# Kernel tuning notes

Measured on AMD Instinct MI355X. Metric: run time of the kernel, lower is better.

The kernel has to match this reference:

```python
import jax, jax.numpy as jnp
import numpy as np

B, S, D, H = 2, 2048, 1024, 16
HD = D // H  # head dim = 64; scale uses sqrt(d_k/num_heads) = sqrt(D/H) since d_k==d_model


def setup_inputs() -> dict:
    key = jax.random.key(0)
    ks = jax.random.split(key, 12)
    s = 1.0 / np.sqrt(D)
    inp = {
        "Q": jax.random.normal(ks[0], (B, S, D), jnp.float32),
        "K": jax.random.normal(ks[1], (B, S, D), jnp.float32),
        "V": jax.random.normal(ks[2], (B, S, D), jnp.float32),
        "mask": jnp.tril(jnp.ones((S, S), jnp.int32))[None, None],  # [1,1,S,S] causal
        "Wq": jax.random.normal(ks[3], (D, D), jnp.float32) * s,
        "bq": jnp.zeros((D,), jnp.float32),
        "Wk": jax.random.normal(ks[4], (D, D), jnp.float32) * s,
        "bk": jnp.zeros((D,), jnp.float32),
        "Wv": jax.random.normal(ks[5], (D, D), jnp.float32) * s,
        "bv": jnp.zeros((D,), jnp.float32),
        "Wo": jax.random.normal(ks[6], (D, D), jnp.float32) * s,
        "bo": jnp.zeros((D,), jnp.float32),
    }
    return inp


def _split_heads(x):
    # [B,S,D] -> [B,H,S,HD]
    b, s, _ = x.shape
    return x.reshape(b, s, H, HD).transpose(0, 2, 1, 3)


def reference(Q, K, V, mask, Wq, bq, Wk, bk, Wv, bv, Wo, bo):
    q = _split_heads(Q @ Wq.T + bq)
    k = _split_heads(K @ Wk.T + bk)
    v = _split_heads(V @ Wv.T + bv)
    scale = 1.0 / jnp.sqrt(jnp.asarray(D / H, q.dtype))  # d_k/num_heads with d_k=d_model
    scores = jnp.einsum('bhqd,bhkd->bhqk', q, k) * scale
    scores = jnp.where(mask == 0, jnp.asarray(-1e9, scores.dtype), scores)
    probs = jax.nn.softmax(scores, axis=-1)
    z = jnp.einsum('bhqk,bhkd->bhqd', probs, v)  # [B,H,S,HD]
    z = z.transpose(0, 2, 1, 3).reshape(Q.shape[0], Q.shape[1], D)
    return z @ Wo.T + bo
```

## Files before the change

### kernel.cpp

```cpp
#include <hip/hip_runtime.h>
#include <hip/hip_bf16.h>

typedef unsigned short u16;
typedef unsigned int u32;
typedef __attribute__((ext_vector_type(2))) unsigned int u32x2;
typedef __attribute__((ext_vector_type(8))) short s16x8;
typedef __attribute__((ext_vector_type(4))) float f32x4;
typedef __attribute__((ext_vector_type(16))) float f32x16;

#define NB 2
#define NH 16
#define NS 2048
#define ND 1024
#define QSCALE 0.1803368801111244f

#define AS1(p) ((const __attribute__((address_space(1))) void*)(p))
#define AS3(p) ((__attribute__((address_space(3))) void*)(p))

__device__ __forceinline__ u16 f2bf(float f) {
  u32 u = __float_as_uint(f);
  u = u + 0x7FFFu + ((u >> 16) & 1u);
  return (u16)(u >> 16);
}

__device__ __forceinline__ float bf2f(u16 h) {
  return __uint_as_float(((u32)h) << 16);
}

__device__ __forceinline__ u32 pkbf(float a, float b) {
  __hip_bfloat162 h = __float22bfloat162_rn(make_float2(a, b));
  union { __hip_bfloat162 h; u32 u; } cv;
  cv.h = h;
  return cv.u;
}

__global__ __launch_bounds__(256) void cvt_kernel(
    const float* __restrict__ q, const float* __restrict__ k,
    const float* __restrict__ v, const float* __restrict__ wq,
    const float* __restrict__ wk, const float* __restrict__ wv,
    const float* __restrict__ wo, u16* __restrict__ Xbf,
    u16* __restrict__ Wbf) {
  const int s = blockIdx.z;
  const size_t M1 = (size_t)1024 * 1024;
  const float* src;
  u16* dst;
  if (s < 4)       { src = q + (size_t)s * M1;        dst = Xbf + (size_t)s * M1; }
  else if (s < 8)  { src = k + (size_t)(s - 4) * M1;  dst = Xbf + (size_t)s * M1; }
  else if (s < 12) { src = v + (size_t)(s - 8) * M1;  dst = Xbf + (size_t)s * M1; }
  else if (s == 12){ src = wq; dst = Wbf; }
  else if (s == 13){ src = wk; dst = Wbf + M1; }
  else if (s == 14){ src = wv; dst = Wbf + 2 * M1; }
  else             { src = wo; dst = Wbf + 3 * M1; }
  const int n4 = 1024 * 1024 / 4;
  for (int i = blockIdx.x * 256 + threadIdx.x; i < n4; i += gridDim.x * 256) {
    float4 a = ((const float4*)src)[i];
    uint2 p;
    p.x = (u32)f2bf(a.x) | ((u32)f2bf(a.y) << 16);
    p.y = (u32)f2bf(a.z) | ((u32)f2bf(a.w) << 16);
    ((uint2*)dst)[i] = p;
  }
}

__global__ __launch_bounds__(256) void gemm_qkv_fast(
    const u16* __restrict__ Xbf, const u16* __restrict__ Wbf,
    const float* __restrict__ bq, const float* __restrict__ bk,
    const float* __restrict__ bv, u16* __restrict__ qh, u16* __restrict__ kh,
    u16* __restrict__ vT) {
  const int which = blockIdx.z;
  const int m0 = blockIdx.y * 128, n0 = blockIdx.x * 128;
  const u16* A = Xbf + (size_t)which * 4096 * 1024;
  const u16* B = Wbf + (size_t)which * 1024 * 1024;
  const float* bias = (which == 0) ? bq : (which == 1) ? bk : bv;
  const int tid = threadIdx.x;
  const int w = tid >> 6, l = tid & 63, lr = l & 15, lg = l >> 4;
  const int wr = (w >> 1) * 64, wc = (w & 1) * 64;

  __shared__ u16 As[2][128 * 32];
  __shared__ u16 Bs[2][128 * 32];

  const int c0 = tid, c1 = 256 + tid;
  const int row0 = c0 >> 2, k40 = (c0 & 3) ^ (row0 & 3);
  const int row1 = c1 >> 2, k41 = (c1 & 3) ^ (row1 & 3);
  const u16* sa0 = A + (size_t)(m0 + row0) * 1024 + k40 * 8;
  const u16* sb0 = B + (size_t)(n0 + row0) * 1024 + k40 * 8;
  const u16* sa1 = A + (size_t)(m0 + row1) * 1024 + k41 * 8;
  const u16* sb1 = B + (size_t)(n0 + row1) * 1024 + k41 * 8;
  const int d0 = (w * 64) * 8, d1 = (256 + w * 64) * 8;

  const f32x4 fzero = {0.f, 0.f, 0.f, 0.f};
  f32x4 acc[4][4];
#pragma unroll
  for (int m = 0; m < 4; ++m)
#pragma unroll
    for (int n = 0; n < 4; ++n) acc[m][n] = fzero;

  auto STAGE = [&](int buf, int k0) {
    __builtin_amdgcn_global_load_lds(AS1(sa0 + k0), AS3(As[buf] + d0), 16, 0, 0);
    __builtin_amdgcn_global_load_lds(AS1(sb0 + k0), AS3(Bs[buf] + d0), 16, 0, 0);
    __builtin_amdgcn_global_load_lds(AS1(sa1 + k0), AS3(As[buf] + d1), 16, 0, 0);
    __builtin_amdgcn_global_load_lds(AS1(sb1 + k0), AS3(Bs[buf] + d1), 16, 0, 0);
  };

  STAGE(0, 0);
  STAGE(1, 32);
  asm volatile("s_waitcnt vmcnt(4)" ::: "memory");
  __builtin_amdgcn_sched_barrier(0);
  __builtin_amdgcn_s_barrier();

  int cur = 0;
  for (int step = 0; step < 32; ++step) {
    s16x8 af[4], bf[4];
#pragma unroll
    for (int m = 0; m < 4; ++m) {
      int row = wr + m * 16 + lr;
      af[m] = *(const s16x8*)(As[cur] + row * 32 + ((lg ^ (row & 3)) * 8));
    }
#pragma unroll
    for (int n = 0; n < 4; ++n) {
      int row = wc + n * 16 + lr;
      bf[n] = *(const s16x8*)(Bs[cur] + row * 32 + ((lg ^ (row & 3)) * 8));
    }
    asm volatile("s_waitcnt lgkmcnt(0)" ::: "memory");
    __builtin_amdgcn_sched_barrier(0);
    __builtin_amdgcn_s_barrier();

    const bool stg = (step + 2 < 32);
    if (stg) STAGE(cur, (step + 2) * 32);

    __builtin_amdgcn_s_setprio(1);
#pragma unroll
    for (int m = 0; m < 4; ++m)
#pragma unroll
      for (int n = 0; n < 4; ++n)
        acc[m][n] = __builtin_amdgcn_mfma_f32_16x16x32_bf16(af[m], bf[n],
                                                            acc[m][n], 0, 0, 0);
    __builtin_amdgcn_s_setprio(0);

    if (stg)
      asm volatile("s_waitcnt vmcnt(4)" ::: "memory");
    else
      asm volatile("s_waitcnt vmcnt(0)" ::: "memory");
    __builtin_amdgcn_sched_barrier(0);
    __builtin_amdgcn_s_barrier();
    cur ^= 1;
  }

#pragma unroll
  for (int m = 0; m < 4; ++m) {
#pragma unroll
    for (int n = 0; n < 4; ++n) {
#pragma unroll
      for (int i = 0; i < 4; ++i) {
        int row = m0 + wr + m * 16 + 4 * lg + i;
        int col = n0 + wc + n * 16 + lr;
        float val = acc[m][n][i] + bias[col];
        if (which == 0) val *= QSCALE;
        int bbi = row >> 11, ss = row & 2047;
        int hhd = col >> 6, hd = col & 63;
        if (which == 0) {
          qh[(((size_t)bbi * NH + hhd) * NS + ss) * 64 + hd] = f2bf(val);
        } else if (which == 1) {
          kh[(((size_t)bbi * NH + hhd) * NS + ss) * 64 + hd] = f2bf(val);
        } else {
          vT[(((size_t)bbi * NH + hhd) * 64 + hd) * NS + ss] = f2bf(val);
        }
      }
    }
  }
}

__global__ __launch_bounds__(256) void gemm_out_fast(
    const u16* __restrict__ zin, const u16* __restrict__ Wbf,
    const float* __restrict__ bo, float* __restrict__ out) {
  const u16* B = Wbf + (size_t)3 * 1024 * 1024;
  const int m0 = blockIdx.y * 128, n0 = blockIdx.x * 128;
  const int tid = threadIdx.x;
  const int w = tid >> 6, l = tid & 63, lr = l & 15, lg = l >> 4;
  const int wr = (w >> 1) * 64, wc = (w & 1) * 64;

  __shared__ u16 As[2][128 * 32];
  __shared__ u16 Bs[2][128 * 32];

  const int c0 = tid, c1 = 256 + tid;
  const int row0 = c0 >> 2, k40 = (c0 & 3) ^ (row0 & 3);
  const int row1 = c1 >> 2, k41 = (c1 & 3) ^ (row1 & 3);
  const u16* sa0 = zin + (size_t)(m0 + row0) * 1024 + k40 * 8;
  const u16* sb0 = B + (size_t)(n0 + row0) * 1024 + k40 * 8;
  const u16* sa1 = zin + (size_t)(m0 + row1) * 1024 + k41 * 8;
  const u16* sb1 = B + (size_t)(n0 + row1) * 1024 + k41 * 8;
  const int d0 = (w * 64) * 8, d1 = (256 + w * 64) * 8;

  const f32x4 fzero = {0.f, 0.f, 0.f, 0.f};
  f32x4 acc[4][4];
#pragma unroll
  for (int m = 0; m < 4; ++m)
#pragma unroll
    for (int n = 0; n < 4; ++n) acc[m][n] = fzero;

  auto STAGE = [&](int buf, int k0) {
    __builtin_amdgcn_global_load_lds(AS1(sa0 + k0), AS3(As[buf] + d0), 16, 0, 0);
    __builtin_amdgcn_global_load_lds(AS1(sb0 + k0), AS3(Bs[buf] + d0), 16, 0, 0);
    __builtin_amdgcn_global_load_lds(AS1(sa1 + k0), AS3(As[buf] + d1), 16, 0, 0);
    __builtin_amdgcn_global_load_lds(AS1(sb1 + k0), AS3(Bs[buf] + d1), 16, 0, 0);
  };

  STAGE(0, 0);
  STAGE(1, 32);
  asm volatile("s_waitcnt vmcnt(4)" ::: "memory");
  __builtin_amdgcn_sched_barrier(0);
  __builtin_amdgcn_s_barrier();

  int cur = 0;
  for (int step = 0; step < 32; ++step) {
    s16x8 af[4], bf[4];
#pragma unroll
    for (int m = 0; m < 4; ++m) {
      int row = wr + m * 16 + lr;
      af[m] = *(const s16x8*)(As[cur] + row * 32 + ((lg ^ (row & 3)) * 8));
    }
#pragma unroll
    for (int n = 0; n < 4; ++n) {
      int row = wc + n * 16 + lr;
      bf[n] = *(const s16x8*)(Bs[cur] + row * 32 + ((lg ^ (row & 3)) * 8));
    }
    asm volatile("s_waitcnt lgkmcnt(0)" ::: "memory");
    __builtin_amdgcn_sched_barrier(0);
    __builtin_amdgcn_s_barrier();

    const bool stg = (step + 2 < 32);
    if (stg) STAGE(cur, (step + 2) * 32);

    __builtin_amdgcn_s_setprio(1);
#pragma unroll
    for (int m = 0; m < 4; ++m)
#pragma unroll
      for (int n = 0; n < 4; ++n)
        acc[m][n] = __builtin_amdgcn_mfma_f32_16x16x32_bf16(af[m], bf[n],
                                                            acc[m][n], 0, 0, 0);
    __builtin_amdgcn_s_setprio(0);

    if (stg)
      asm volatile("s_waitcnt vmcnt(4)" ::: "memory");
    else
      asm volatile("s_waitcnt vmcnt(0)" ::: "memory");
    __builtin_amdgcn_sched_barrier(0);
    __builtin_amdgcn_s_barrier();
    cur ^= 1;
  }

#pragma unroll
  for (int m = 0; m < 4; ++m)
#pragma unroll
    for (int n = 0; n < 4; ++n)
#pragma unroll
      for (int i = 0; i < 4; ++i) {
        int row = m0 + wr + m * 16 + 4 * lg + i;
        int col = n0 + wc + n * 16 + lr;
        out[(size_t)row * 1024 + col] = acc[m][n][i] + bo[col];
      }
}

__device__ __forceinline__ void stage64(const u16* __restrict__ kh,
                                        const u16* __restrict__ vT, int bh,
                                        int t, int tid, int w, u16* kbase,
                                        u16* vbase) {
#pragma unroll
  for (int i = 0; i < 2; ++i) {
    int c = i * 256 + tid;
    int row = c >> 3, k8 = (c & 7) ^ (row & 7);
    const u16* sk = kh + ((size_t)bh * NS + t * 64 + row) * 64 + k8 * 8;
    const u16* sv = vT + ((size_t)bh * 64 + row) * NS + t * 64 + k8 * 8;
    u16* dk = kbase + (i * 256 + w * 64) * 8;
    u16* dv = vbase + (i * 256 + w * 64) * 8;
    __builtin_amdgcn_global_load_lds(AS1(sk), AS3(dk), 16, 0, 0);
    __builtin_amdgcn_global_load_lds(AS1(sv), AS3(dv), 16, 0, 0);
  }
}

__global__ __launch_bounds__(256) void attn_split_kernel(
    const u16* __restrict__ qh, const u16* __restrict__ kh,
    const u16* __restrict__ vT, u16* __restrict__ Opart,
    float* __restrict__ Mpart, float* __restrict__ Lpart) {
  const int f = blockIdx.x;
  const int bh = f & 31;
  const int pp = f >> 5;
  const int tid = threadIdx.x;
  const int w = tid >> 6, l = tid & 63;
  const int ql = l & 31, hi = l >> 5, hi8 = hi * 8;

  __shared__ u16 smem[3][2][64][64];

#pragma unroll 1
  for (int c = 0; c < 2; ++c) {
    const int band = c ? (15 - pp) : pp;
    const int t0 = c ? (16 - pp) : 0;
    const int t1 = c ? (32 - 2 * pp) : (pp + 1);
    const int nt = t1 - t0;
    const int q0w = band * 128 + w * 32;

    s16x8 qf[4];
    {
      const u16* qp = qh + ((size_t)bh * NS + q0w + ql) * 64 + hi8;
#pragma unroll
      for (int st = 0; st < 4; ++st) qf[st] = *(const s16x8*)(qp + st * 16);
    }

    f32x16 o0 = {0, 0, 0, 0, 0, 0, 0, 0, 0, 0, 0, 0, 0, 0, 0, 0};
    f32x16 o1 = {0, 0, 0, 0, 0, 0, 0, 0, 0, 0, 0, 0, 0, 0, 0, 0};
    float m_run = -1e30f, l_run = 0.f;

    __syncthreads();
    stage64(kh, vT, bh, t0, tid, w, &smem[t0 % 3][0][0][0],
            &smem[t0 % 3][1][0][0]);
    if (nt > 1)
      stage64(kh, vT, bh, t0 + 1, tid, w, &smem[(t0 + 1) % 3][0][0][0],
              &smem[(t0 + 1) % 3][1][0][0]);
    if (nt > 1)
      asm volatile("s_waitcnt vmcnt(4)" ::: "memory");
    else
      asm volatile("s_waitcnt vmcnt(0)" ::: "memory");
    __builtin_amdgcn_sched_barrier(0);
    __builtin_amdgcn_s_barrier();

    for (int t = t0; t < t1; ++t) {
      const bool stg = (t + 2 < t1);
      if (stg)
        stage64(kh, vT, bh, t + 2, tid, w, &smem[(t + 2) % 3][0][0][0],
                &smem[(t + 2) % 3][1][0][0]);
      const u16* kp = &smem[t % 3][0][0][0];
      const u16* vp = &smem[t % 3][1][0][0];

      const int kvg0 = t * 64, kvg1 = t * 64 + 32;
      if (kvg0 <= q0w) {
        f32x16 s0 = {0, 0, 0, 0, 0, 0, 0, 0, 0, 0, 0, 0, 0, 0, 0, 0};
        f32x16 s1 = {0, 0, 0, 0, 0, 0, 0, 0, 0, 0, 0, 0, 0, 0, 0, 0};
        const int kr0 = ql, kr1 = 32 + ql;
        __builtin_amdgcn_s_setprio(1);
#pragma unroll
        for (int st = 0; st < 4; ++st) {
          s16x8 ak = *(const s16x8*)(kp + kr0 * 64 +
                                     (((st * 2 + hi) ^ (kr0 & 7)) * 8));
          s0 = __builtin_amdgcn_mfma_f32_32x32x16_bf16(ak, qf[st], s0, 0, 0, 0);
        }
        if (kvg1 <= q0w) {
#pragma unroll
          for (int st = 0; st < 4; ++st) {
            s16x8 ak = *(const s16x8*)(kp + kr1 * 64 +
                                       (((st * 2 + hi) ^ (kr1 & 7)) * 8));
            s1 = __builtin_amdgcn_mfma_f32_32x32x16_bf16(ak, qf[st], s1, 0, 0,
                                                         0);
          }
        }
        __builtin_amdgcn_s_setprio(0);

        if (kvg0 == q0w) {
#pragma unroll
          for (int r = 0; r < 16; ++r) {
            int kvloc = (r & 3) + 8 * (r >> 2) + 4 * hi;
            if (kvloc > ql) s0[r] = -1e30f;
          }
        }
        if (kvg1 > q0w) {
#pragma unroll
          for (int r = 0; r < 16; ++r) s1[r] = -1e30f;
        } else if (kvg1 == q0w) {
#pragma unroll
          for (int r = 0; r < 16; ++r) {
            int kvloc = (r & 3) + 8 * (r >> 2) + 4 * hi;
            if (kvloc > ql) s1[r] = -1e30f;
          }
        }

        float mr[16];
#pragma unroll
        for (int r = 0; r < 16; ++r) mr[r] = fmaxf(s0[r], s1[r]);
#pragma unroll
        for (int off = 8; off; off >>= 1)
#pragma unroll
          for (int r = 0; r < 8; ++r)
            if (r < off) mr[r] = fmaxf(mr[r], mr[r + off]);
        float mx = mr[0];
        {
          u32x2 rm = __builtin_amdgcn_permlane32_swap(
              __float_as_uint(mx), __float_as_uint(mx), 0, 0);
          mx = fmaxf(__uint_as_float(rm.x), __uint_as_float(rm.y));
        }

        if (!__all(mx - m_run <= 8.0f)) {
          float mnew = fmaxf(m_run, mx);
          float fs = __builtin_amdgcn_exp2f(m_run - mnew);
#pragma unroll
          for (int r = 0; r < 16; ++r) {
            o0[r] *= fs;
            o1[r] *= fs;
          }
          l_run *= fs;
          m_run = mnew;
        }

        float ps = 0.f;
        u32 pk0[8], pk1[8];
#pragma unroll
        for (int tt = 0; tt < 8; ++tt) {
          float a = __builtin_amdgcn_exp2f(s0[2 * tt] - m_run);
          float b = __builtin_amdgcn_exp2f(s0[2 * tt + 1] - m_run);
          ps += a + b;
          pk0[tt] = pkbf(a, b);
        }
#pragma unroll
        for (int tt = 0; tt < 8; ++tt) {
          float a = __builtin_amdgcn_exp2f(s1[2 * tt] - m_run);
          float b = __builtin_amdgcn_exp2f(s1[2 * tt + 1] - m_run);
          ps += a + b;
          pk1[tt] = pkbf(a, b);
        }
        {
          u32x2 rp = __builtin_amdgcn_permlane32_swap(
              __float_as_uint(ps), __float_as_uint(ps), 0, 0);
          ps = __uint_as_float(rp.x) + __uint_as_float(rp.y);
        }
        l_run += ps;

        u32x2 e0 = __builtin_amdgcn_permlane32_swap(pk0[0], pk0[2], 0, 0);
        u32x2 e1 = __builtin_amdgcn_permlane32_swap(pk0[1], pk0[3], 0, 0);
        u32x2 e2 = __builtin_amdgcn_permlane32_swap(pk0[4], pk0[6], 0, 0);
        u32x2 e3 = __builtin_amdgcn_permlane32_swap(pk0[5], pk0[7], 0, 0);
        u32x2 e4 = __builtin_amdgcn_permlane32_swap(pk1[0], pk1[2], 0, 0);
        u32x2 e5 = __builtin_amdgcn_permlane32_swap(pk1[1], pk1[3], 0, 0);
        u32x2 e6 = __builtin_amdgcn_permlane32_swap(pk1[4], pk1[6], 0, 0);
        u32x2 e7 = __builtin_amdgcn_permlane32_swap(pk1[5], pk1[7], 0, 0);
        union { u32 u[4]; s16x8 h; } pf[4];
        pf[0].u[0] = e0.x; pf[0].u[1] = e1.x; pf[0].u[2] = e0.y; pf[0].u[3] = e1.y;
        pf[1].u[0] = e2.x; pf[1].u[1] = e3.x; pf[1].u[2] = e2.y; pf[1].u[3] = e3.y;
        pf[2].u[0] = e4.x; pf[2].u[1] = e5.x; pf[2].u[2] = e4.y; pf[2].u[3] = e5.y;
        pf[3].u[0] = e6.x; pf[3].u[1] = e7.x; pf[3].u[2] = e6.y; pf[3].u[3] = e7.y;

        __builtin_amdgcn_s_setprio(1);
#pragma unroll
        for (int ks = 0; ks < 4; ++ks) {
          int ch = ks * 2 + hi;
          s16x8 av0 = *(const s16x8*)(vp + ql * 64 + ((ch ^ (ql & 7)) * 8));
          s16x8 av1 =
              *(const s16x8*)(vp + (32 + ql) * 64 + ((ch ^ (ql & 7)) * 8));
          o0 = __builtin_amdgcn_mfma_f32_32x32x16_bf16(av0, pf[ks].h, o0, 0, 0,
                                                       0);
          o1 = __builtin_amdgcn_mfma_f32_32x32x16_bf16(av1, pf[ks].h, o1, 0, 0,
                                                       0);
        }
        __builtin_amdgcn_s_setprio(0);
      }

      if (stg)
        asm volatile("s_waitcnt vmcnt(4)" ::: "memory");
      else
        asm volatile("s_waitcnt vmcnt(0)" ::: "memory");
      __builtin_amdgcn_sched_barrier(0);
      __builtin_amdgcn_s_barrier();
    }

    u16* Zw = &smem[0][0][0][0] + w * (32 * 72);
#pragma unroll
    for (int r = 0; r < 16; r += 2) {
      int d0 = (r & 3) + 8 * (r >> 2) + 4 * hi;
      *(u32*)&Zw[ql * 72 + d0]      = pkbf(o0[r], o0[r + 1]);
      *(u32*)&Zw[ql * 72 + 32 + d0] = pkbf(o1[r], o1[r + 1]);
    }
    if (hi == 0) {
      size_t mix = ((size_t)c * 32 + bh) * NS + q0w + ql;
      Mpart[mix] = m_run;
      Lpart[mix] = l_run;
    }
#pragma unroll
    for (int i = 0; i < 4; ++i) {
      int cid = i * 64 + l;
      int row = cid >> 3, c8 = (cid & 7) * 8;
      s16x8 vv = *(const s16x8*)&Zw[row * 72 + c8];
      *(s16x8*)(Opart + (((size_t)c * 32 + bh) * NS + q0w + row) * 64 + c8) =
          vv;
    }
  }
}

__global__ __launch_bounds__(256) void attn_combine_kernel(
    const u16* __restrict__ Opart, const float* __restrict__ Mpart,
    const float* __restrict__ Lpart, u16* __restrict__ z) {
  const int tok = blockIdx.x;
  const int bb = tok >> 11, ss = tok & 2047;
  const int t = threadIdx.x;
  const int d4 = t * 4;
  const int hh = d4 >> 6;
  const size_t qix = ((size_t)bb * NH + hh) * NS + ss;
  const size_t stride = (size_t)32 * NS;

  float m0 = Mpart[qix], l0 = Lpart[qix];
  float m1 = Mpart[qix + stride], l1 = Lpart[qix + stride];
  float mm = fmaxf(m0, m1);
  float w0 = __builtin_amdgcn_exp2f(m0 - mm);
  float w1 = __builtin_amdgcn_exp2f(m1 - mm);
  float inv = 1.f / (w0 * l0 + w1 * l1);
  w0 *= inv;
  w1 *= inv;

  size_t ob = qix * 64 + (d4 & 63);
  uint2 a = *(const uint2*)(Opart + ob);
  uint2 b = *(const uint2*)(Opart + ob + stride * 64);

  float z0 = bf2f((u16)(a.x & 0xffff)) * w0 + bf2f((u16)(b.x & 0xffff)) * w1;
  float z1 = bf2f((u16)(a.x >> 16)) * w0 + bf2f((u16)(b.x >> 16)) * w1;
  float z2 = bf2f((u16)(a.y & 0xffff)) * w0 + bf2f((u16)(b.y & 0xffff)) * w1;
  float z3 = bf2f((u16)(a.y >> 16)) * w0 + bf2f((u16)(b.y >> 16)) * w1;

  uint2 p;
  p.x = pkbf(z0, z1);
  p.y = pkbf(z2, z3);
  *(uint2*)(z + ((size_t)bb * NS + ss) * ND + d4) = p;
}

__global__ __launch_bounds__(128) void attn_kernel(
    const u16* __restrict__ qh, const u16* __restrict__ kh,
    const u16* __restrict__ vT, u16* __restrict__ z) {
  const int f = blockIdx.x;
  const int bh = f & 31;
  const int j0 = (f >> 5) & 7;
  const int g = f >> 8;
  const int mb = 2 * j0;
  const int m =
      (g == 0) ? mb : (g == 1) ? mb + 1 : (g == 2) ? 30 - mb : 31 - mb;
  const int bb = bh >> 4, hh = bh & 15;
  const int tid = threadIdx.x;
  const int w = tid >> 6, l = tid & 63;
  const int ql = l & 31, hi = l >> 5, hi8 = hi * 8;
  const int q0w = m * 64 + w * 32;

  __shared__ u16 smem[2][2][64][64];

  s16x8 qf[4];
  {
    const u16* qp = qh + ((size_t)bh * NS + q0w + ql) * 64 + hi8;
#pragma unroll
    for (int st = 0; st < 4; ++st) qf[st] = *(const s16x8*)(qp + st * 16);
  }

  f32x16 o0 = {0, 0, 0, 0, 0, 0, 0, 0, 0, 0, 0, 0, 0, 0, 0, 0};
  f32x16 o1 = {0, 0, 0, 0, 0, 0, 0, 0, 0, 0, 0, 0, 0, 0, 0, 0};
  float m_run = -1e30f, l_run = 0.f;

  const int ntiles = m + 1;

#pragma unroll
  for (int i = 0; i < 4; ++i) {
    int c = i * 128 + tid;
    int row = c >> 3, k8 = (c & 7) ^ (row & 7);
    const u16* sk = kh + ((size_t)bh * NS + row) * 64 + k8 * 8;
    const u16* sv = vT + ((size_t)bh * 64 + row) * NS + k8 * 8;
    u16* dk = &smem[0][0][0][0] + (i * 128 + w * 64) * 8;
    u16* dv = &smem[0][1][0][0] + (i * 128 + w * 64) * 8;
    __builtin_amdgcn_global_load_lds(AS1(sk), AS3(dk), 16, 0, 0);
    __builtin_amdgcn_global_load_lds(AS1(sv), AS3(dv), 16, 0, 0);
  }
  __syncthreads();

  for (int t = 0; t < ntiles; ++t) {
    if (t + 1 < ntiles) {
      int b1 = (t + 1) & 1;
#pragma unroll
      for (int i = 0; i < 4; ++i) {
        int c = i * 128 + tid;
        int row = c >> 3, k8 = (c & 7) ^ (row & 7);
        const u16* sk =
            kh + ((size_t)bh * NS + (t + 1) * 64 + row) * 64 + k8 * 8;
        const u16* sv =
            vT + ((size_t)bh * 64 + row) * NS + (t + 1) * 64 + k8 * 8;
        u16* dk = &smem[b1][0][0][0] + (i * 128 + w * 64) * 8;
        u16* dv = &smem[b1][1][0][0] + (i * 128 + w * 64) * 8;
        __builtin_amdgcn_global_load_lds(AS1(sk), AS3(dk), 16, 0, 0);
        __builtin_amdgcn_global_load_lds(AS1(sv), AS3(dv), 16, 0, 0);
      }
    }
    const u16* kp = &smem[t & 1][0][0][0];
    const u16* vp = &smem[t & 1][1][0][0];

#pragma unroll
    for (int sub = 0; sub < 2; ++sub) {
      const int kvg = t * 64 + sub * 32;
      if (kvg > q0w) continue;
      const bool masked = (kvg == q0w);

      const int kr = sub * 32 + ql;
      f32x16 s = {0, 0, 0, 0, 0, 0, 0, 0, 0, 0, 0, 0, 0, 0, 0, 0};
#pragma unroll
      for (int st = 0; st < 4; ++st) {
        s16x8 ak = *(const s16x8*)(kp + kr * 64 +
                                   (((st * 2 + hi) ^ (kr & 7)) * 8));
        s = __builtin_amdgcn_mfma_f32_32x32x16_bf16(ak, qf[st], s, 0, 0, 0);
      }

      float sv_[16];
#pragma unroll
      for (int r = 0; r < 16; ++r) {
        float x = s[r];
        if (masked) {
          int kvloc = (r & 3) + 8 * (r >> 2) + 4 * hi;
          if (kvloc > ql) x = -1e30f;
        }
        sv_[r] = x;
      }

      float mx = sv_[0];
#pragma unroll
      for (int r = 1; r < 16; ++r) mx = fmaxf(mx, sv_[r]);
      {
        u32x2 rm = __builtin_amdgcn_permlane32_swap(__float_as_uint(mx),
                                                    __float_as_uint(mx), 0, 0);
        mx = fmaxf(__uint_as_float(rm.x), __uint_as_float(rm.y));
      }

      if (__any(mx > m_run)) {
        float mnew = fmaxf(m_run, mx);
        float fs = __builtin_amdgcn_exp2f(m_run - mnew);
#pragma unroll
        for (int r = 0; r < 16; ++r) {
          o0[r] *= fs;
          o1[r] *= fs;
        }
        l_run *= fs;
        m_run = mnew;
      }

      float ps = 0.f;
      u32 pk[8];
#pragma unroll
      for (int tt = 0; tt < 8; ++tt) {
        float a = __builtin_amdgcn_exp2f(sv_[2 * tt] - m_run);
        float b = __builtin_amdgcn_exp2f(sv_[2 * tt + 1] - m_run);
        ps += a + b;
        pk[tt] = pkbf(a, b);
      }
      {
        u32x2 rp = __builtin_amdgcn_permlane32_swap(__float_as_uint(ps),
                                                    __float_as_uint(ps), 0, 0);
        ps = __uint_as_float(rp.x) + __uint_as_float(rp.y);
      }
      l_run += ps;

      u32x2 e0 = __builtin_amdgcn_permlane32_swap(pk[0], pk[2], 0, 0);
      u32x2 e1 = __builtin_amdgcn_permlane32_swap(pk[1], pk[3], 0, 0);
      u32x2 e2 = __builtin_amdgcn_permlane32_swap(pk[4], pk[6], 0, 0);
      u32x2 e3 = __builtin_amdgcn_permlane32_swap(pk[5], pk[7], 0, 0);
      union { u32 u[4]; s16x8 h; } pf0, pf1;
      pf0.u[0] = e0.x; pf0.u[1] = e1.x; pf0.u[2] = e0.y; pf0.u[3] = e1.y;
      pf1.u[0] = e2.x; pf1.u[1] = e3.x; pf1.u[2] = e2.y; pf1.u[3] = e3.y;

#pragma unroll
      for (int k2 = 0; k2 < 2; ++k2) {
        s16x8 pa = (k2 == 0) ? pf0.h : pf1.h;
        int ch = sub * 4 + k2 * 2 + hi;
        s16x8 av0 = *(const s16x8*)(vp + ql * 64 + ((ch ^ (ql & 7)) * 8));
        s16x8 av1 =
            *(const s16x8*)(vp + (32 + ql) * 64 + ((ch ^ (ql & 7)) * 8));
        o0 = __builtin_amdgcn_mfma_f32_32x32x16_bf16(av0, pa, o0, 0, 0, 0);
        o1 = __builtin_amdgcn_mfma_f32_32x32x16_bf16(av1, pa, o1, 0, 0, 0);
      }
    }
    __syncthreads();
  }

  float inv = 1.f / l_run;
  u16* Zw = &smem[0][0][0][0] + w * (32 * 72);
#pragma unroll
  for (int r = 0; r < 16; r += 2) {
    int d0 = (r & 3) + 8 * (r >> 2) + 4 * hi;
    *(u32*)&Zw[ql * 72 + d0]      = pkbf(o0[r] * inv, o0[r + 1] * inv);
    *(u32*)&Zw[ql * 72 + 32 + d0] = pkbf(o1[r] * inv, o1[r + 1] * inv);
  }
#pragma unroll
  for (int i = 0; i < 4; ++i) {
    int cid = i * 64 + l;
    int row = cid >> 3, c8 = (cid & 7) * 8;
    s16x8 vv = *(const s16x8*)&Zw[row * 72 + c8];
    *(s16x8*)(z + ((size_t)bb * NS + q0w + row) * ND + hh * 64 + c8) = vv;
  }
}

__global__ __launch_bounds__(256) void proj_qkv_kernel(
    const float* __restrict__ Qin, const float* __restrict__ Kin,
    const float* __restrict__ Vin,
    const float* __restrict__ Wq, const float* __restrict__ bq,
    const float* __restrict__ Wk, const float* __restrict__ bk,
    const float* __restrict__ Wv, const float* __restrict__ bv,
    u16* __restrict__ qh, u16* __restrict__ kh, u16* __restrict__ vT) {
  const int which = blockIdx.z;
  const float* X = (which == 0) ? Qin : (which == 1) ? Kin : Vin;
  const float* W = (which == 0) ? Wq : (which == 1) ? Wk : Wv;
  const float* bias = (which == 0) ? bq : (which == 1) ? bk : bv;

  const int m0 = blockIdx.y * 128, n0 = blockIdx.x * 128;
  const int tid = threadIdx.x;
  const int w = tid >> 6, l = tid & 63, lr = l & 15, lg = l >> 4;
  const int wr = (w >> 1) * 64, wc = (w & 1) * 64;

  __shared__ u16 As[128][40];
  __shared__ u16 Bs[128][40];

  const f32x4 fzero = {0.f, 0.f, 0.f, 0.f};
  f32x4 acc[4][4];
#pragma unroll
  for (int m = 0; m < 4; ++m)
#pragma unroll
    for (int n = 0; n < 4; ++n) acc[m][n] = fzero;

  for (int k0 = 0; k0 < 1024; k0 += 32) {
#pragma unroll
    for (int i = 0; i < 4; ++i) {
      int idx = tid + i * 256;
      int row = idx >> 3, c4 = (idx & 7) * 4;
      float4 a = *(const float4*)(X + (size_t)(m0 + row) * 1024 + k0 + c4);
      *(u32*)&As[row][c4]     = (u32)f2bf(a.x) | ((u32)f2bf(a.y) << 16);
      *(u32*)&As[row][c4 + 2] = (u32)f2bf(a.z) | ((u32)f2bf(a.w) << 16);
      float4 b = *(const float4*)(W + (size_t)(n0 + row) * 1024 + k0 + c4);
      *(u32*)&Bs[row][c4]     = (u32)f2bf(b.x) | ((u32)f2bf(b.y) << 16);
      *(u32*)&Bs[row][c4 + 2] = (u32)f2bf(b.z) | ((u32)f2bf(b.w) << 16);
    }
    __syncthreads();
    s16x8 af[4], bf[4];
#pragma unroll
    for (int m = 0; m < 4; ++m)
      af[m] = *(const s16x8*)&As[wr + m * 16 + lr][lg * 8];
#pragma unroll
    for (int n = 0; n < 4; ++n)
      bf[n] = *(const s16x8*)&Bs[wc + n * 16 + lr][lg * 8];
#pragma unroll
    for (int m = 0; m < 4; ++m)
#pragma unroll
      for (int n = 0; n < 4; ++n)
        acc[m][n] = __builtin_amdgcn_mfma_f32_16x16x32_bf16(af[m], bf[n],
                                                            acc[m][n], 0, 0, 0);
    __syncthreads();
  }

  u16* dst01 = (which == 0) ? qh : kh;
#pragma unroll
  for (int m = 0; m < 4; ++m) {
#pragma unroll
    for (int n = 0; n < 4; ++n) {
#pragma unroll
      for (int i = 0; i < 4; ++i) {
        int row = m0 + wr + m * 16 + 4 * lg + i;
        int col = n0 + wc + n * 16 + lr;
        float val = acc[m][n][i] + bias[col];
        if (which == 0) val *= QSCALE;
        int bbi = row >> 11, ss = row & 2047;
        int hhd = col >> 6, hd = col & 63;
        if (which < 2) {
          dst01[(((size_t)bbi * NH + hhd) * NS + ss) * 64 + hd] = f2bf(val);
        } else {
          vT[(((size_t)bbi * NH + hhd) * 64 + hd) * NS + ss] = f2bf(val);
        }
      }
    }
  }
}

__global__ __launch_bounds__(256) void proj_out_kernel(
    const u16* __restrict__ zin, const float* __restrict__ Wo,
    const float* __restrict__ bo, float* __restrict__ out) {
  const int m0 = blockIdx.y * 128, n0 = blockIdx.x * 128;
  const int tid = threadIdx.x;
  const int w = tid >> 6, l = tid & 63, lr = l & 15, lg = l >> 4;
  const int wr = (w >> 1) * 64, wc = (w & 1) * 64;

  __shared__ u16 As[128][40];
  __shared__ u16 Bs[128][40];

  const f32x4 fzero = {0.f, 0.f, 0.f, 0.f};
  f32x4 acc[4][4];
#pragma unroll
  for (int m = 0; m < 4; ++m)
#pragma unroll
    for (int n = 0; n < 4; ++n) acc[m][n] = fzero;

  for (int k0 = 0; k0 < 1024; k0 += 32) {
#pragma unroll
    for (int i = 0; i < 2; ++i) {
      int idx = tid + i * 256;
      int row = idx >> 2, c8 = (idx & 3) * 8;
      *(s16x8*)&As[row][c8] =
          *(const s16x8*)(zin + (size_t)(m0 + row) * 1024 + k0 + c8);
    }
#pragma unroll
    for (int i = 0; i < 4; ++i) {
      int idx = tid + i * 256;
      int row = idx >> 3, c4 = (idx & 7) * 4;
      float4 b = *(const float4*)(Wo + (size_t)(n0 + row) * 1024 + k0 + c4);
      *(u32*)&Bs[row][c4]     = (u32)f2bf(b.x) | ((u32)f2bf(b.y) << 16);
      *(u32*)&Bs[row][c4 + 2] = (u32)f2bf(b.z) | ((u32)f2bf(b.w) << 16);
    }
    __syncthreads();
    s16x8 af[4], bf[4];
#pragma unroll
    for (int m = 0; m < 4; ++m)
      af[m] = *(const s16x8*)&As[wr + m * 16 + lr][lg * 8];
#pragma unroll
    for (int n = 0; n < 4; ++n)
      bf[n] = *(const s16x8*)&Bs[wc + n * 16 + lr][lg * 8];
#pragma unroll
    for (int m = 0; m < 4; ++m)
#pragma unroll
      for (int n = 0; n < 4; ++n)
        acc[m][n] = __builtin_amdgcn_mfma_f32_16x16x32_bf16(af[m], bf[n],
                                                            acc[m][n], 0, 0, 0);
    __syncthreads();
  }

#pragma unroll
  for (int m = 0; m < 4; ++m)
#pragma unroll
    for (int n = 0; n < 4; ++n)
#pragma unroll
      for (int i = 0; i < 4; ++i) {
        int row = m0 + wr + m * 16 + 4 * lg + i;
        int col = n0 + wc + n * 16 + lr;
        out[(size_t)row * 1024 + col] = acc[m][n][i] + bo[col];
      }
}

extern "C" void kernel_launch(void* const* d_in, const int* in_sizes, int n_in,
                              void* d_out, int out_size, void* d_ws,
                              size_t ws_size, hipStream_t stream) {
  const float* Q = (const float*)d_in[0];
  const float* K = (const float*)d_in[1];
  const float* V = (const float*)d_in[2];
  const float* Wq = (const float*)d_in[4];
  const float* bq = (const float*)d_in[5];
  const float* Wk = (const float*)d_in[6];
  const float* bk = (const float*)d_in[7];
  const float* Wv = (const float*)d_in[8];
  const float* bv = (const float*)d_in[9];
  const float* Wo = (const float*)d_in[10];
  const float* bo = (const float*)d_in[11];
  float* out = (float*)d_out;

  const size_t M1 = (size_t)1024 * 1024;
  u16* base = (u16*)d_ws;

  if (ws_size >= (size_t)58720256) {
    u16* Wbf = base;
    u16* qh = base + 4 * M1;
    u16* zz = qh;
    u16* kh = base + 8 * M1;
    u16* vT = base + 12 * M1;
    u16* Xbf = base + 16 * M1;
    u16* Opart = base + 16 * M1;
    float* Mpart = (float*)(base + 24 * M1);
    float* Lpart = (float*)(base + 24 * M1 + 256 * 1024);

    cvt_kernel<<<dim3(128, 1, 16), 256, 0, stream>>>(Q, K, V, Wq, Wk, Wv, Wo,
                                                     Xbf, Wbf);
    gemm_qkv_fast<<<dim3(8, 32, 3), 256, 0, stream>>>(Xbf, Wbf, bq, bk, bv,
                                                      qh, kh, vT);
    attn_split_kernel<<<dim3(512), 256, 0, stream>>>(qh, kh, vT, Opart, Mpart,
                                                     Lpart);
    attn_combine_kernel<<<dim3(4096), 256, 0, stream>>>(Opart, Mpart, Lpart,
                                                        zz);
    gemm_out_fast<<<dim3(8, 32), 256, 0, stream>>>(zz, Wbf, bo, out);
  } else {
    u16* qh = base;
    u16* kh = base + 4 * M1;
    u16* vT = base + 8 * M1;
    u16* zz = base + 12 * M1;
    proj_qkv_kernel<<<dim3(8, 32, 3), 256, 0, stream>>>(Q, K, V, Wq, bq, Wk,
                                                        bk, Wv, bv, qh, kh, vT);
    attn_kernel<<<dim3(1024), 128, 0, stream>>>(qh, kh, vT, zz);
    proj_out_kernel<<<dim3(8, 32), 256, 0, stream>>>(zz, Wo, bo, out);
  }
}
```

Before: 134.1 us.

## Software-pipeline QK^T of next tile with softmax/PV of previous tile

Restructures the attention inner loop so that each iteration computes the QK^T scores for tile it while doing softmax and PV for tile it-1. The LDS ring grows from three to four K/V buffers so the previous tile's V stays resident while new tiles are staged. The aim is to overlap MFMA score work with the exp/reduction work, at the cost of extra live registers (two more 16-float accumulators), more shared memory per block and an extra barrier before the epilogue.

```diff
diff --git a/kernel.cpp b/kernel.cpp
--- a/kernel.cpp
+++ b/kernel.cpp
@@ -288,7 +288,7 @@
   const int w = tid >> 6, l = tid & 63;
   const int ql = l & 31, hi = l >> 5, hi8 = hi * 8;
 
-  __shared__ u16 smem[3][2][64][64];
+  __shared__ u16 smem[4][2][64][64];
 
 #pragma unroll 1
   for (int c = 0; c < 2; ++c) {
@@ -310,11 +310,11 @@
     float m_run = -1e30f, l_run = 0.f;
 
     __syncthreads();
-    stage64(kh, vT, bh, t0, tid, w, &smem[t0 % 3][0][0][0],
-            &smem[t0 % 3][1][0][0]);
+    stage64(kh, vT, bh, t0, tid, w, &smem[t0 & 3][0][0][0],
+            &smem[t0 & 3][1][0][0]);
     if (nt > 1)
-      stage64(kh, vT, bh, t0 + 1, tid, w, &smem[(t0 + 1) % 3][0][0][0],
-              &smem[(t0 + 1) % 3][1][0][0]);
+      stage64(kh, vT, bh, t0 + 1, tid, w, &smem[(t0 + 1) & 3][0][0][0],
+              &smem[(t0 + 1) & 3][1][0][0]);
     if (nt > 1)
       asm volatile("s_waitcnt vmcnt(4)" ::: "memory");
     else
@@ -322,58 +322,70 @@
     __builtin_amdgcn_sched_barrier(0);
     __builtin_amdgcn_s_barrier();
 
-    for (int t = t0; t < t1; ++t) {
-      const bool stg = (t + 2 < t1);
+    f32x16 p0 = o0, p1 = o0;
+    bool pvalid = false;
+    int pt = t0;
+
+    for (int it = t0; it <= t1; ++it) {
+      f32x16 sq0 = {0, 0, 0, 0, 0, 0, 0, 0, 0, 0, 0, 0, 0, 0, 0, 0};
+      f32x16 sq1 = {0, 0, 0, 0, 0, 0, 0, 0, 0, 0, 0, 0, 0, 0, 0, 0};
+      bool qvalid = false;
+      if (it < t1) {
+        const u16* kp = &smem[it & 3][0][0][0];
+        const int kvg0 = it * 64, kvg1 = it * 64 + 32;
+        if (kvg0 <= q0w) {
+          qvalid = true;
+          const int kr0 = ql, kr1 = 32 + ql;
+          __builtin_amdgcn_s_setprio(1);
+#pragma unroll
+          for (int st = 0; st < 4; ++st) {
+            s16x8 ak = *(const s16x8*)(kp + kr0 * 64 +
+                                       (((st * 2 + hi) ^ (kr0 & 7)) * 8));
+            sq0 = __builtin_amdgcn_mfma_f32_32x32x16_bf16(ak, qf[st], sq0, 0,
+                                                          0, 0);
+          }
+          if (kvg1 <= q0w) {
+#pragma unroll
+            for (int st = 0; st < 4; ++st) {
+              s16x8 ak = *(const s16x8*)(kp + kr1 * 64 +
+                                         (((st * 2 + hi) ^ (kr1 & 7)) * 8));
+              sq1 = __builtin_amdgcn_mfma_f32_32x32x16_bf16(ak, qf[st], sq1, 0,
+                                                            0, 0);
+            }
+          }
+          __builtin_amdgcn_s_setprio(0);
+
+          if (kvg0 == q0w) {
+#pragma unroll
+            for (int r = 0; r < 16; ++r) {
+              int kvloc = (r & 3) + 8 * (r >> 2) + 4 * hi;
+              if (kvloc > ql) sq0[r] = -1e30f;
+            }
+          }
+          if (kvg1 > q0w) {
+#pragma unroll
+            for (int r = 0; r < 16; ++r) sq1[r] = -1e30f;
+          } else if (kvg1 == q0w) {
+#pragma unroll
+            for (int r = 0; r < 16; ++r) {
+              int kvloc = (r & 3) + 8 * (r >> 2) + 4 * hi;
+              if (kvloc > ql) sq1[r] = -1e30f;
+            }
+          }
+        }
+      }
+
+      const bool stg = (it + 2 < t1);
       if (stg)
-        stage64(kh, vT, bh, t + 2, tid, w, &smem[(t + 2) % 3][0][0][0],
-                &smem[(t + 2) % 3][1][0][0]);
-      const u16* kp = &smem[t % 3][0][0][0];
-      const u16* vp = &smem[t % 3][1][0][0];
-
-      const int kvg0 = t * 64, kvg1 = t * 64 + 32;
-      if (kvg0 <= q0w) {
-        f32x16 s0 = {0, 0, 0, 0, 0, 0, 0, 0, 0, 0, 0, 0, 0, 0, 0, 0};
-        f32x16 s1 = {0, 0, 0, 0, 0, 0, 0, 0, 0, 0, 0, 0, 0, 0, 0, 0};
-        const int kr0 = ql, kr1 = 32 + ql;
-        __builtin_amdgcn_s_setprio(1);
-#pragma unroll
-        for (int st = 0; st < 4; ++st) {
-          s16x8 ak = *(const s16x8*)(kp + kr0 * 64 +
-                                     (((st * 2 + hi) ^ (kr0 & 7)) * 8));
-          s0 = __builtin_amdgcn_mfma_f32_32x32x16_bf16(ak, qf[st], s0, 0, 0, 0);
-        }
-        if (kvg1 <= q0w) {
-#pragma unroll
-          for (int st = 0; st < 4; ++st) {
-            s16x8 ak = *(const s16x8*)(kp + kr1 * 64 +
-                                       (((st * 2 + hi) ^ (kr1 & 7)) * 8));
-            s1 = __builtin_amdgcn_mfma_f32_32x32x16_bf16(ak, qf[st], s1, 0, 0,
-                                                         0);
-          }
-        }
-        __builtin_amdgcn_s_setprio(0);
-
-        if (kvg0 == q0w) {
-#pragma unroll
-          for (int r = 0; r < 16; ++r) {
-            int kvloc = (r & 3) + 8 * (r >> 2) + 4 * hi;
-            if (kvloc > ql) s0[r] = -1e30f;
-          }
-        }
-        if (kvg1 > q0w) {
-#pragma unroll
-          for (int r = 0; r < 16; ++r) s1[r] = -1e30f;
-        } else if (kvg1 == q0w) {
-#pragma unroll
-          for (int r = 0; r < 16; ++r) {
-            int kvloc = (r & 3) + 8 * (r >> 2) + 4 * hi;
-            if (kvloc > ql) s1[r] = -1e30f;
-          }
-        }
+        stage64(kh, vT, bh, it + 2, tid, w, &smem[(it + 2) & 3][0][0][0],
+                &smem[(it + 2) & 3][1][0][0]);
+
+      if (pvalid) {
+        const u16* vp = &smem[pt & 3][1][0][0];
 
         float mr[16];
 #pragma unroll
-        for (int r = 0; r < 16; ++r) mr[r] = fmaxf(s0[r], s1[r]);
+        for (int r = 0; r < 16; ++r) mr[r] = fmaxf(p0[r], p1[r]);
 #pragma unroll
         for (int off = 8; off; off >>= 1)
 #pragma unroll
@@ -402,15 +414,15 @@
         u32 pk0[8], pk1[8];
 #pragma unroll
         for (int tt = 0; tt < 8; ++tt) {
-          float a = __builtin_amdgcn_exp2f(s0[2 * tt] - m_run);
-          float b = __builtin_amdgcn_exp2f(s0[2 * tt + 1] - m_run);
+          float a = __builtin_amdgcn_exp2f(p0[2 * tt] - m_run);
+          float b = __builtin_amdgcn_exp2f(p0[2 * tt + 1] - m_run);
           ps += a + b;
           pk0[tt] = pkbf(a, b);
         }
 #pragma unroll
         for (int tt = 0; tt < 8; ++tt) {
-          float a = __builtin_amdgcn_exp2f(s1[2 * tt] - m_run);
-          float b = __builtin_amdgcn_exp2f(s1[2 * tt + 1] - m_run);
+          float a = __builtin_amdgcn_exp2f(p1[2 * tt] - m_run);
+          float b = __builtin_amdgcn_exp2f(p1[2 * tt + 1] - m_run);
           ps += a + b;
           pk1[tt] = pkbf(a, b);
         }
@@ -450,13 +462,22 @@
         __builtin_amdgcn_s_setprio(0);
       }
 
-      if (stg)
-        asm volatile("s_waitcnt vmcnt(4)" ::: "memory");
-      else
-        asm volatile("s_waitcnt vmcnt(0)" ::: "memory");
-      __builtin_amdgcn_sched_barrier(0);
-      __builtin_amdgcn_s_barrier();
-    }
+      if (it < t1) {
+        if (stg)
+          asm volatile("s_waitcnt vmcnt(4)" ::: "memory");
+        else
+          asm volatile("s_waitcnt vmcnt(0)" ::: "memory");
+        __builtin_amdgcn_sched_barrier(0);
+        __builtin_amdgcn_s_barrier();
+      }
+
+      p0 = sq0;
+      p1 = sq1;
+      pvalid = qvalid;
+      pt = it;
+    }
+
+    __syncthreads();
 
     u16* Zw = &smem[0][0][0][0] + w * (32 * 72);
 #pragma unroll
```

Measured after the change: 136.9 us. +2.1%, slower.
